# Optimization experiments

Hardware: AMD Instinct MI355X
Metric: run time of the kernel (lower is better)

Reference implementation:

```python
import jax, jax.numpy as jnp
import numpy as np

N_POINTS = 100000
N_PAIRS = 50000   # pairs per kernel offset
K_OFFSETS = 27    # 3^3 kernel offsets for 3D kernel_size=3
C = 128


def setup_inputs() -> dict:
    key = jax.random.key(0)
    ks = jax.random.split(key, 7)
    features = jax.random.normal(ks[0], (N_POINTS, C), dtype=jnp.float32)
    in_map = jax.random.randint(ks[1], (K_OFFSETS, N_PAIRS), 0, N_POINTS)
    out_map = jax.random.randint(ks[2], (K_OFFSETS, N_PAIRS), 0, N_POINTS)
    # scale weights so two stacked convs stay numerically tame in fp32
    W0 = jax.random.normal(ks[3], (K_OFFSETS, C, C), dtype=jnp.float32) * 0.05
    b0 = jax.random.normal(ks[4], (C,), dtype=jnp.float32)
    W1 = jax.random.normal(ks[5], (K_OFFSETS, C, C), dtype=jnp.float32) * 0.05
    b1 = jax.random.normal(ks[6], (C,), dtype=jnp.float32)
    return {"features": features, "in_map": in_map, "out_map": out_map,
            "W0": W0, "b0": b0, "W1": W1, "b1": b1}


def _sparse_conv(x, W, b, in_map, out_map, n_out):
    """Minkowski-style sparse conv: gather -> per-offset matmul -> scatter-add.
    x: [N, C], W: [K, C, C], in_map/out_map: [K, P]."""
    gathered = x[in_map]                                  # [K, P, C]
    msg = jnp.einsum('kpc,kcd->kpd', gathered, W)         # [K, P, C]
    y = jax.ops.segment_sum(msg.reshape(-1, msg.shape[-1]),
                            out_map.reshape(-1),
                            num_segments=n_out)           # [N, C]
    return y + b


def reference(features, in_map, out_map, W0, b0, W1, b1):
    n = features.shape[0]
    out = jax.nn.relu(_sparse_conv(features, W0, b0, in_map, out_map, n))
    out = _sparse_conv(out, W1, b1, in_map, out_map, n)
    return out + features
```

## Files before the change

kernel.cpp:

```cpp
#include <hip/hip_runtime.h>

#define N_POINTS 100000
#define N_PAIRS  50000
#define K_OFFSETS 27
#define C 128
#define WPAD 136
#define CAP 48

#define NQ 4
#define QPTS 25000
#define MSGCAP 360448
#define GX 110

#define CSR_GROUPS 8
#define CSR_BPG 128

typedef __attribute__((ext_vector_type(8))) short short8;
typedef __attribute__((ext_vector_type(4))) float floatx4;

__device__ inline unsigned short f2bf(float f) {
  unsigned int u = __float_as_uint(f);
  return (unsigned short)((u + 0x7FFFu + ((u >> 16) & 1u)) >> 16);
}
__device__ inline float bf2f(unsigned int lo16) {
  return __uint_as_float(lo16 << 16);
}

__global__ __launch_bounds__(256) void prep_w_kernel(
    const float* __restrict__ W0, const float* __restrict__ W1,
    unsigned short* __restrict__ WT0, unsigned short* __restrict__ WT1) {
  int i = blockIdx.x * 256 + threadIdx.x;
  const int per = K_OFFSETS * C * C;
  if (i >= 2 * per) return;
  const float* W = (i < per) ? W0 : W1;
  unsigned short* WT = (i < per) ? WT0 : WT1;
  int r = (i < per) ? i : i - per;
  int k = r / (C * C);
  int q = r % (C * C);
  int d = q / C;
  int c = q % C;
  WT[k * C * C + d * C + c] = f2bf(W[k * C * C + c * C + d]);
}

__global__ __launch_bounds__(256) void prep_x_kernel(
    const float* __restrict__ features, const float* __restrict__ b0,
    unsigned short* __restrict__ xb, float* __restrict__ out, int write_out) {
  int i = (blockIdx.x * 256 + threadIdx.x) * 4;
  if (i >= N_POINTS * C) return;
  float4 f = *(const float4*)&features[i];
  ushort4 u;
  u.x = f2bf(f.x); u.y = f2bf(f.y); u.z = f2bf(f.z); u.w = f2bf(f.w);
  *(ushort4*)&xb[i] = u;
  if (write_out) {
    float4 b = *(const float4*)&b0[i & 127];
    *(float4*)&out[i] = b;
  }
}

__global__ __launch_bounds__(256) void zero_meta_kernel(
    int* __restrict__ counts, int* __restrict__ counts_hk) {
  int i = blockIdx.x * 256 + threadIdx.x;
  if (i < N_POINTS) counts[i] = 0;
  if (i < NQ * K_OFFSETS) counts_hk[i] = 0;
}

__global__ __launch_bounds__(256) void count_hk_kernel(
    const int* __restrict__ out_map, int* __restrict__ counts_hk) {
  __shared__ int hist[NQ * K_OFFSETS];
  if (threadIdx.x < NQ * K_OFFSETS) hist[threadIdx.x] = 0;
  __syncthreads();
  const int total4 = K_OFFSETS * N_PAIRS / 4;
  for (int i4 = blockIdx.x * 256 + (int)threadIdx.x; i4 < total4; i4 += 256 * 256) {
    int4 o4 = *(const int4*)&out_map[i4 * 4];
    int o[4] = {o4.x, o4.y, o4.z, o4.w};
    int k = (i4 * 4) / N_PAIRS;
#pragma unroll
    for (int j = 0; j < 4; ++j) atomicAdd(&hist[(o[j] / QPTS) * K_OFFSETS + k], 1);
  }
  __syncthreads();
  if (threadIdx.x < NQ * K_OFFSETS)
    atomicAdd(&counts_hk[threadIdx.x], hist[threadIdx.x]);
}

__global__ void scan_kernel(const int* __restrict__ counts_hk,
                            int* __restrict__ base_hk, int* __restrict__ cursor_hk) {
  if (threadIdx.x < NQ) {
    int h = threadIdx.x;
    int run = 0;
    for (int k = 0; k < K_OFFSETS; ++k) {
      base_hk[h * K_OFFSETS + k] = run;
      cursor_hk[h * K_OFFSETS + k] = run;
      run += (counts_hk[h * K_OFFSETS + k] + 31) & ~31;
    }
  }
}

__global__ __launch_bounds__(256) void build2_kernel(
    const int* __restrict__ out_map, const int* __restrict__ in_map,
    int* __restrict__ counts, int* __restrict__ idxbuf,
    int* __restrict__ cursor_hk, int* __restrict__ pairlist) {
  __shared__ int histA[K_OFFSETS];
  __shared__ int kbase[K_OFFSETS];
  const int grp = blockIdx.x & (CSR_GROUPS - 1);
  const int blk = blockIdx.x >> 3;
  const int h = grp >> 1;
  const int lo = grp * (N_POINTS / CSR_GROUPS);
  const int hi = lo + (N_POINTS / CSR_GROUPS);
  if (threadIdx.x < K_OFFSETS) histA[threadIdx.x] = 0;
  __syncthreads();
  const int total4 = K_OFFSETS * N_PAIRS / 4;
  for (int i4 = blk * 256 + (int)threadIdx.x; i4 < total4; i4 += CSR_BPG * 256) {
    int4 o4 = *(const int4*)&out_map[i4 * 4];
    int o[4] = {o4.x, o4.y, o4.z, o4.w};
    int k = (i4 * 4) / N_PAIRS;
#pragma unroll
    for (int j = 0; j < 4; ++j)
      if (o[j] >= lo && o[j] < hi) atomicAdd(&histA[k], 1);
  }
  __syncthreads();
  if (threadIdx.x < K_OFFSETS) {
    kbase[threadIdx.x] =
        atomicAdd(&cursor_hk[h * K_OFFSETS + threadIdx.x], histA[threadIdx.x]);
    histA[threadIdx.x] = 0;
  }
  __syncthreads();
  for (int i4 = blk * 256 + (int)threadIdx.x; i4 < total4; i4 += CSR_BPG * 256) {
    int4 o4 = *(const int4*)&out_map[i4 * 4];
    int4 n4 = *(const int4*)&in_map[i4 * 4];
    int o[4] = {o4.x, o4.y, o4.z, o4.w};
    int n[4] = {n4.x, n4.y, n4.z, n4.w};
    int k = (i4 * 4) / N_PAIRS;
#pragma unroll
    for (int j = 0; j < 4; ++j) {
      if (o[j] >= lo && o[j] < hi) {
        int pk = atomicAdd(&histA[k], 1);
        int slot = kbase[k] + pk;
        pairlist[h * MSGCAP + slot] = n[j];
        int pos = atomicAdd(&counts[o[j]], 1);
        if (pos < CAP) idxbuf[o[j] * CAP + pos] = slot;
      }
    }
  }
}

__global__ __launch_bounds__(256, 4) void conv2_kernel(
    const unsigned short* __restrict__ xin, const unsigned short* __restrict__ wbt,
    const int* __restrict__ counts_hk, const int* __restrict__ base_hk,
    const int* __restrict__ pairlist, unsigned short* __restrict__ msg2, int h) {
  __shared__ unsigned short Wlds[C * WPAD];
  const int k = blockIdx.y;
  const int cnt = counts_hk[h * K_OFFSETS + k];
  const int cpad = (cnt + 31) & ~31;
  const int off0 = blockIdx.x * 128;
  if (off0 >= cpad) return;
  const int kb = base_hk[h * K_OFFSETS + k];
  const int tid = threadIdx.x;

  const unsigned short* wk = wbt + k * C * C;
#pragma unroll
  for (int it = 0; it < 8; ++it) {
    int t = tid + it * 256;
    int row = t >> 4;
    int col = (t & 15) << 3;
    *(uint4*)&Wlds[row * WPAD + col] = *(const uint4*)&wk[row * C + col];
  }
  __syncthreads();

  const int wave = tid >> 6;
  const int lane = tid & 63;
  const int l15 = lane & 15;
  const int kg = lane >> 4;
  const int ws0 = off0 + wave * 32;
  if (ws0 >= cpad) return;

  const int s0 = kb + ws0;
  const int plbase = h * MSGCAP;
  const int n0 = pairlist[plbase + s0 + l15] & 0x1FFFF;
  const int n1 = pairlist[plbase + s0 + 16 + l15] & 0x1FFFF;
  const unsigned short* arow0 = xin + (size_t)n0 * C + kg * 8;
  const unsigned short* arow1 = xin + (size_t)n1 * C + kg * 8;

  floatx4 acc0[8], acc1[8];
#pragma unroll
  for (int nt = 0; nt < 8; ++nt) {
    acc0[nt] = (floatx4){0.f, 0.f, 0.f, 0.f};
    acc1[nt] = (floatx4){0.f, 0.f, 0.f, 0.f};
  }
#pragma unroll
  for (int kk = 0; kk < 4; ++kk) {
    short8 a0 = *(const short8*)(arow0 + kk * 32);
    short8 a1 = *(const short8*)(arow1 + kk * 32);
    const unsigned short* bbase = &Wlds[l15 * WPAD + kk * 32 + kg * 8];
#pragma unroll
    for (int nt = 0; nt < 8; ++nt) {
      short8 b = *(const short8*)(bbase + nt * 16 * WPAD);
      acc0[nt] = __builtin_amdgcn_mfma_f32_16x16x32_bf16(a0, b, acc0[nt], 0, 0, 0);
      acc1[nt] = __builtin_amdgcn_mfma_f32_16x16x32_bf16(a1, b, acc1[nt], 0, 0, 0);
    }
  }
#pragma unroll
  for (int i = 0; i < 4; ++i) {
    {
      unsigned short* row = msg2 + (size_t)(s0 + kg * 4 + i) * C;
      uint4 v;
      v.x = (unsigned int)f2bf(acc0[0][i]) | ((unsigned int)f2bf(acc0[1][i]) << 16);
      v.y = (unsigned int)f2bf(acc0[2][i]) | ((unsigned int)f2bf(acc0[3][i]) << 16);
      v.z = (unsigned int)f2bf(acc0[4][i]) | ((unsigned int)f2bf(acc0[5][i]) << 16);
      v.w = (unsigned int)f2bf(acc0[6][i]) | ((unsigned int)f2bf(acc0[7][i]) << 16);
      *(uint4*)(row + l15 * 8) = v;
    }
    {
      unsigned short* row = msg2 + (size_t)(s0 + 16 + kg * 4 + i) * C;
      uint4 v;
      v.x = (unsigned int)f2bf(acc1[0][i]) | ((unsigned int)f2bf(acc1[1][i]) << 16);
      v.y = (unsigned int)f2bf(acc1[2][i]) | ((unsigned int)f2bf(acc1[3][i]) << 16);
      v.z = (unsigned int)f2bf(acc1[4][i]) | ((unsigned int)f2bf(acc1[5][i]) << 16);
      v.w = (unsigned int)f2bf(acc1[6][i]) | ((unsigned int)f2bf(acc1[7][i]) << 16);
      *(uint4*)(row + l15 * 8) = v;
    }
  }
}

__global__ __launch_bounds__(256) void gather2_kernel(
    const unsigned short* __restrict__ msg2, const int* __restrict__ counts,
    const int* __restrict__ idxbuf, const float* __restrict__ bias,
    const float* __restrict__ features, float* __restrict__ out,
    unsigned short* __restrict__ x1b, int h, int layer) {
  __shared__ int elds[4][64];
  const int wave = threadIdx.x >> 6;
  const int lane = threadIdx.x & 63;
  const int oi = h * QPTS + blockIdx.x * 4 + wave;

  const int c0 = ((2 * lane) & 7) * 16 + (lane >> 2);
  const int c1 = c0 + 16;
  const size_t base = (size_t)oi * C;

  float a0, a1;
  if (layer == 0) { a0 = bias[c0]; a1 = bias[c1]; }
  else            { a0 = bias[c0] + features[base + c0];
                    a1 = bias[c1] + features[base + c1]; }

  int cnt = counts[oi]; if (cnt > CAP) cnt = CAP;
  if (lane < cnt) elds[wave][lane] = idxbuf[oi * CAP + lane];
  __syncthreads();

  const unsigned short* mb = msg2 + 2 * lane;
  int t = 0;
  for (; t + 4 <= cnt; t += 4) {
    int f0 = elds[wave][t];
    int f1 = elds[wave][t + 1];
    int f2 = elds[wave][t + 2];
    int f3 = elds[wave][t + 3];
    unsigned int v0 = *(const unsigned int*)(mb + (size_t)f0 * C);
    unsigned int v1 = *(const unsigned int*)(mb + (size_t)f1 * C);
    unsigned int v2 = *(const unsigned int*)(mb + (size_t)f2 * C);
    unsigned int v3 = *(const unsigned int*)(mb + (size_t)f3 * C);
    a0 += bf2f(v0 & 0xffffu) + bf2f(v1 & 0xffffu) + bf2f(v2 & 0xffffu) + bf2f(v3 & 0xffffu);
    a1 += bf2f(v0 >> 16) + bf2f(v1 >> 16) + bf2f(v2 >> 16) + bf2f(v3 >> 16);
  }
  for (; t < cnt; ++t) {
    int f0 = elds[wave][t];
    unsigned int v = *(const unsigned int*)(mb + (size_t)f0 * C);
    a0 += bf2f(v & 0xffffu);
    a1 += bf2f(v >> 16);
  }

  if (layer == 0) {
    x1b[base + c0] = f2bf(fmaxf(a0, 0.f));
    x1b[base + c1] = f2bf(fmaxf(a1, 0.f));
  } else {
    out[base + c0] = a0;
    out[base + c1] = a1;
  }
}

__global__ __launch_bounds__(256) void mid_kernel(
    const float* __restrict__ features, const float* __restrict__ b1,
    float* __restrict__ out, unsigned short* __restrict__ x1b) {
  int i = (blockIdx.x * 256 + threadIdx.x) * 4;
  if (i >= N_POINTS * C) return;
  float4 y = *(const float4*)&out[i];
  ushort4 u;
  u.x = f2bf(fmaxf(y.x, 0.f));
  u.y = f2bf(fmaxf(y.y, 0.f));
  u.z = f2bf(fmaxf(y.z, 0.f));
  u.w = f2bf(fmaxf(y.w, 0.f));
  *(ushort4*)&x1b[i] = u;
  float4 f = *(const float4*)&features[i];
  float4 b = *(const float4*)&b1[i & 127];
  float4 o;
  o.x = f.x + b.x; o.y = f.y + b.y; o.z = f.z + b.z; o.w = f.w + b.w;
  *(float4*)&out[i] = o;
}

__global__ __launch_bounds__(256, 4) void conv_atomic_kernel(
    const unsigned short* __restrict__ xb, const unsigned short* __restrict__ wbt,
    const int* __restrict__ in_map, const int* __restrict__ out_map,
    float* __restrict__ out) {
  __shared__ unsigned short Wlds[C * WPAD];
  const int k = blockIdx.y;
  const int pairBase = blockIdx.x * 64;
  const int tid = threadIdx.x;
  const unsigned short* wk = wbt + k * C * C;
#pragma unroll
  for (int it = 0; it < 8; ++it) {
    int t = tid + it * 256;
    int row = t >> 4;
    int col = (t & 15) << 3;
    *(uint4*)&Wlds[row * WPAD + col] = *(const uint4*)&wk[row * C + col];
  }
  __syncthreads();
  const int wave = tid >> 6;
  const int lane = tid & 63;
  const int l15 = lane & 15;
  const int kg = lane >> 4;
  const int pair0 = pairBase + wave * 16;
  const int prA = pair0 + l15;
  const int inIdx = (prA < N_PAIRS) ? in_map[k * N_PAIRS + prA] : 0;
  const unsigned short* arow = xb + (size_t)inIdx * C + kg * 8;
  floatx4 acc[8];
#pragma unroll
  for (int nt = 0; nt < 8; ++nt) acc[nt] = (floatx4){0.f, 0.f, 0.f, 0.f};
#pragma unroll
  for (int kk = 0; kk < 4; ++kk) {
    short8 a = *(const short8*)(arow + kk * 32);
    const unsigned short* bbase = &Wlds[l15 * WPAD + kk * 32 + kg * 8];
#pragma unroll
    for (int nt = 0; nt < 8; ++nt) {
      short8 b = *(const short8*)(bbase + nt * 16 * WPAD);
      acc[nt] = __builtin_amdgcn_mfma_f32_16x16x32_bf16(a, b, acc[nt], 0, 0, 0);
    }
  }
#pragma unroll
  for (int i = 0; i < 4; ++i) {
    int pr = pair0 + kg * 4 + i;
    if (pr < N_PAIRS) {
      int oi = out_map[k * N_PAIRS + pr];
      float* orow = out + (size_t)oi * C + l15;
#pragma unroll
      for (int nt = 0; nt < 8; ++nt) atomicAdd(orow + nt * 16, acc[nt][i]);
    }
  }
}

extern "C" void kernel_launch(void* const* d_in, const int* in_sizes, int n_in,
                              void* d_out, int out_size, void* d_ws, size_t ws_size,
                              hipStream_t stream) {
  const float* features = (const float*)d_in[0];
  const int* in_map     = (const int*)d_in[1];
  const int* out_map    = (const int*)d_in[2];
  const float* W0       = (const float*)d_in[3];
  const float* b0       = (const float*)d_in[4];
  const float* W1       = (const float*)d_in[5];
  const float* b1       = (const float*)d_in[6];
  float* out = (float*)d_out;

  char* ws = (char*)d_ws;
  unsigned short* xb  = (unsigned short*)(ws);
  unsigned short* x1b = (unsigned short*)(ws + 25600000);
  unsigned short* WT0 = (unsigned short*)(ws + 51200000);
  unsigned short* WT1 = (unsigned short*)(ws + 52084736);
  int* counts         = (int*)(ws + 52969472);
  int* counts_hk      = (int*)(ws + 53369856);
  int* base_hk        = (int*)(ws + 53370368);
  int* cursor_hk      = (int*)(ws + 53370880);
  int* pairlist       = (int*)(ws + 53371392);
  int* idxbuf         = (int*)(ws + 59138560);
  unsigned short* msg2 = (unsigned short*)(ws + 78338560);

  const int use2 = (ws_size >= 170613248ULL) ? 1 : 0;

  prep_w_kernel<<<(2 * K_OFFSETS * C * C + 255) / 256, 256, 0, stream>>>(W0, W1, WT0, WT1);
  prep_x_kernel<<<(N_POINTS * C / 4 + 255) / 256, 256, 0, stream>>>(
      features, b0, xb, out, use2 ? 0 : 1);

  if (use2) {
    zero_meta_kernel<<<(N_POINTS + 255) / 256, 256, 0, stream>>>(counts, counts_hk);
    count_hk_kernel<<<256, 256, 0, stream>>>(out_map, counts_hk);
    scan_kernel<<<1, 64, 0, stream>>>(counts_hk, base_hk, cursor_hk);
    build2_kernel<<<CSR_GROUPS * CSR_BPG, 256, 0, stream>>>(
        out_map, in_map, counts, idxbuf, cursor_hk, pairlist);

    for (int layer = 0; layer < 2; ++layer) {
      const unsigned short* xin = layer ? x1b : xb;
      const unsigned short* wt  = layer ? WT1 : WT0;
      const float* bias         = layer ? b1  : b0;
      for (int h = 0; h < NQ; ++h) {
        dim3 cgrid(GX, K_OFFSETS);
        conv2_kernel<<<cgrid, 256, 0, stream>>>(
            xin, wt, counts_hk, base_hk, pairlist, msg2, h);
        gather2_kernel<<<QPTS / 4, 256, 0, stream>>>(
            msg2, counts, idxbuf, bias, features, out, x1b, h, layer);
      }
    }
  } else {
    dim3 cgrid((N_PAIRS + 63) / 64, K_OFFSETS);
    conv_atomic_kernel<<<cgrid, 256, 0, stream>>>(xb, WT0, in_map, out_map, out);
    mid_kernel<<<(N_POINTS * C / 4 + 255) / 256, 256, 0, stream>>>(features, b1, out, x1b);
    conv_atomic_kernel<<<cgrid, 256, 0, stream>>>(x1b, WT1, in_map, out_map, out);
  }
}
```

Baseline: 671.6 us.

## Batch two output quarters per conv/gather launch and use nontemporal map loads

When the workspace is large enough, conv2 and gather2 now process two output-point quarters per launch. Each quarter writes to its own message buffer slab, indexed by blockIdx.z. This halves the number of launches and makes each launch's grid larger, which should cut per-launch tail and idle time, at the cost of a larger workspace. It also shrinks MSGCAP, shifts the buffer offsets to match, and switches the out_map/in_map loads in the histogram and CSR-build kernels to nontemporal loads.

```diff
diff --git a/kernel.cpp b/kernel.cpp
--- a/kernel.cpp
+++ b/kernel.cpp
@@ -9,7 +9,7 @@
 
 #define NQ 4
 #define QPTS 25000
-#define MSGCAP 360448
+#define MSGCAP 344064
 #define GX 110
 
 #define CSR_GROUPS 8
@@ -17,6 +17,7 @@
 
 typedef __attribute__((ext_vector_type(8))) short short8;
 typedef __attribute__((ext_vector_type(4))) float floatx4;
+typedef __attribute__((ext_vector_type(4))) int intx4;
 
 __device__ inline unsigned short f2bf(float f) {
   unsigned int u = __float_as_uint(f);
@@ -71,7 +72,7 @@
   __syncthreads();
   const int total4 = K_OFFSETS * N_PAIRS / 4;
   for (int i4 = blockIdx.x * 256 + (int)threadIdx.x; i4 < total4; i4 += 256 * 256) {
-    int4 o4 = *(const int4*)&out_map[i4 * 4];
+    intx4 o4 = __builtin_nontemporal_load((const intx4*)&out_map[i4 * 4]);
     int o[4] = {o4.x, o4.y, o4.z, o4.w};
     int k = (i4 * 4) / N_PAIRS;
 #pragma unroll
@@ -110,7 +111,7 @@
   __syncthreads();
   const int total4 = K_OFFSETS * N_PAIRS / 4;
   for (int i4 = blk * 256 + (int)threadIdx.x; i4 < total4; i4 += CSR_BPG * 256) {
-    int4 o4 = *(const int4*)&out_map[i4 * 4];
+    intx4 o4 = __builtin_nontemporal_load((const intx4*)&out_map[i4 * 4]);
     int o[4] = {o4.x, o4.y, o4.z, o4.w};
     int k = (i4 * 4) / N_PAIRS;
 #pragma unroll
@@ -125,8 +126,8 @@
   }
   __syncthreads();
   for (int i4 = blk * 256 + (int)threadIdx.x; i4 < total4; i4 += CSR_BPG * 256) {
-    int4 o4 = *(const int4*)&out_map[i4 * 4];
-    int4 n4 = *(const int4*)&in_map[i4 * 4];
+    intx4 o4 = __builtin_nontemporal_load((const intx4*)&out_map[i4 * 4]);
+    intx4 n4 = __builtin_nontemporal_load((const intx4*)&in_map[i4 * 4]);
     int o[4] = {o4.x, o4.y, o4.z, o4.w};
     int n[4] = {n4.x, n4.y, n4.z, n4.w};
     int k = (i4 * 4) / N_PAIRS;
@@ -146,8 +147,9 @@
 __global__ __launch_bounds__(256, 4) void conv2_kernel(
     const unsigned short* __restrict__ xin, const unsigned short* __restrict__ wbt,
     const int* __restrict__ counts_hk, const int* __restrict__ base_hk,
-    const int* __restrict__ pairlist, unsigned short* __restrict__ msg2, int h) {
+    const int* __restrict__ pairlist, unsigned short* __restrict__ msg2, int h0) {
   __shared__ unsigned short Wlds[C * WPAD];
+  const int h = h0 + blockIdx.z;
   const int k = blockIdx.y;
   const int cnt = counts_hk[h * K_OFFSETS + k];
   const int cpad = (cnt + 31) & ~31;
@@ -198,10 +200,11 @@
       acc1[nt] = __builtin_amdgcn_mfma_f32_16x16x32_bf16(a1, b, acc1[nt], 0, 0, 0);
     }
   }
+  unsigned short* mz = msg2 + (size_t)blockIdx.z * MSGCAP * C;
 #pragma unroll
   for (int i = 0; i < 4; ++i) {
     {
-      unsigned short* row = msg2 + (size_t)(s0 + kg * 4 + i) * C;
+      unsigned short* row = mz + (size_t)(s0 + kg * 4 + i) * C;
       uint4 v;
       v.x = (unsigned int)f2bf(acc0[0][i]) | ((unsigned int)f2bf(acc0[1][i]) << 16);
       v.y = (unsigned int)f2bf(acc0[2][i]) | ((unsigned int)f2bf(acc0[3][i]) << 16);
@@ -210,7 +213,7 @@
       *(uint4*)(row + l15 * 8) = v;
     }
     {
-      unsigned short* row = msg2 + (size_t)(s0 + 16 + kg * 4 + i) * C;
+      unsigned short* row = mz + (size_t)(s0 + 16 + kg * 4 + i) * C;
       uint4 v;
       v.x = (unsigned int)f2bf(acc1[0][i]) | ((unsigned int)f2bf(acc1[1][i]) << 16);
       v.y = (unsigned int)f2bf(acc1[2][i]) | ((unsigned int)f2bf(acc1[3][i]) << 16);
@@ -225,11 +228,13 @@
     const unsigned short* __restrict__ msg2, const int* __restrict__ counts,
     const int* __restrict__ idxbuf, const float* __restrict__ bias,
     const float* __restrict__ features, float* __restrict__ out,
-    unsigned short* __restrict__ x1b, int h, int layer) {
+    unsigned short* __restrict__ x1b, int h0, int layer) {
   __shared__ int elds[4][64];
   const int wave = threadIdx.x >> 6;
   const int lane = threadIdx.x & 63;
-  const int oi = h * QPTS + blockIdx.x * 4 + wave;
+  const int z = blockIdx.x / (QPTS / 4);
+  const int bx = blockIdx.x - z * (QPTS / 4);
+  const int oi = (h0 + z) * QPTS + bx * 4 + wave;
 
   const int c0 = ((2 * lane) & 7) * 16 + (lane >> 2);
   const int c1 = c0 + 16;
@@ -244,7 +249,7 @@
   if (lane < cnt) elds[wave][lane] = idxbuf[oi * CAP + lane];
   __syncthreads();
 
-  const unsigned short* mb = msg2 + 2 * lane;
+  const unsigned short* mb = msg2 + (size_t)z * MSGCAP * C + 2 * lane;
   int t = 0;
   for (; t + 4 <= cnt; t += 4) {
     int f0 = elds[wave][t];
@@ -365,10 +370,11 @@
   int* base_hk        = (int*)(ws + 53370368);
   int* cursor_hk      = (int*)(ws + 53370880);
   int* pairlist       = (int*)(ws + 53371392);
-  int* idxbuf         = (int*)(ws + 59138560);
-  unsigned short* msg2 = (unsigned short*)(ws + 78338560);
-
-  const int use2 = (ws_size >= 170613248ULL) ? 1 : 0;
+  int* idxbuf         = (int*)(ws + 58876416);
+  unsigned short* msg2 = (unsigned short*)(ws + 78076416);
+
+  const int use2  = (ws_size >= 166156800ULL) ? 1 : 0;
+  const int BATCH = (ws_size >= 254237184ULL) ? 2 : 1;
 
   prep_w_kernel<<<(2 * K_OFFSETS * C * C + 255) / 256, 256, 0, stream>>>(W0, W1, WT0, WT1);
   prep_x_kernel<<<(N_POINTS * C / 4 + 255) / 256, 256, 0, stream>>>(
@@ -385,12 +391,12 @@
       const unsigned short* xin = layer ? x1b : xb;
       const unsigned short* wt  = layer ? WT1 : WT0;
       const float* bias         = layer ? b1  : b0;
-      for (int h = 0; h < NQ; ++h) {
-        dim3 cgrid(GX, K_OFFSETS);
+      for (int h0 = 0; h0 < NQ; h0 += BATCH) {
+        dim3 cgrid(GX, K_OFFSETS, BATCH);
         conv2_kernel<<<cgrid, 256, 0, stream>>>(
-            xin, wt, counts_hk, base_hk, pairlist, msg2, h);
-        gather2_kernel<<<QPTS / 4, 256, 0, stream>>>(
-            msg2, counts, idxbuf, bias, features, out, x1b, h, layer);
+            xin, wt, counts_hk, base_hk, pairlist, msg2, h0);
+        gather2_kernel<<<(QPTS / 4) * BATCH, 256, 0, stream>>>(
+            msg2, counts, idxbuf, bias, features, out, x1b, h0, layer);
       }
     }
   } else {
```

Measured after the change: 675.9 us. Within noise of the previous version (+0.6%).
